# Kernel optimization log

Measured on AMD Instinct MI355X. Metric: run time of the kernel, lower is better.

## Reference

```python
import jax, jax.numpy as jnp
import numpy as np

CLASS_NUM = 4            # number of positive classes
NUM_CLASSES = CLASS_NUM + 1  # last column is the negative class
W_P = 4.0
EPS = 1e-9
THR = 0.5


def setup_inputs() -> dict:
    key = jax.random.key(0)
    k1, k2 = jax.random.split(key)
    N = 4_000_000
    x = jax.random.normal(k1, (N, NUM_CLASSES), dtype=jnp.float32)
    t = jax.random.randint(k2, (N,), 0, NUM_CLASSES)
    return {"x": x, "t": t}


def _conf_mpu_loss(x, t):
    N = x.shape[0]
    p = jax.nn.softmax(x, axis=1)                       # [N, C]
    log_pneg = jnp.log(p[:, -1] + EPS)                  # [N]

    ones = jnp.ones((N,), dtype=jnp.float32)
    counts = jax.ops.segment_sum(ones, t, num_segments=NUM_CLASSES)  # per-class counts
    prior = counts[:CLASS_NUM] / N                      # empirical priors (positive classes)

    # loss_per_class: sum over samples with t==c of -log(p[n,c]+eps)
    logp_t = jnp.log(jnp.take_along_axis(p, t[:, None], axis=1)[:, 0] + EPS)
    class_losses = jax.ops.segment_sum(-logp_t, t, num_segments=NUM_CLASSES)

    # loss_per_class_neg: sum over samples with t==i (i positive) of -log(p_neg+eps)
    loss_neg = jax.ops.segment_sum(-log_pneg, t, num_segments=NUM_CLASSES)[:CLASS_NUM]

    # conf_loss_per_class
    conf = []
    for i in range(CLASS_NUM):
        mask = (p[:, i] > THR) & (t == i)
        nsel = jnp.sum(mask.astype(jnp.float32))
        li = jnp.sum(jnp.where(mask, -log_pneg / p[:, i], 0.0))
        conf.append(li / jnp.maximum(nsel, 1.0))        # li==0 when nsel==0
    mask_n = jnp.all(p <= THR, axis=1) & (t == CLASS_NUM)
    li_n = jnp.sum(jnp.where(mask_n, -log_pneg, 0.0))
    conf_neg = li_n / jnp.maximum(counts[CLASS_NUM], 1.0)  # li_n==0 when no selection
    conf_pos = jnp.stack(conf)                          # [CLASS_NUM]

    denom = jnp.maximum(1.0, counts[:CLASS_NUM])
    risk1 = jnp.sum(prior * class_losses[:CLASS_NUM] / denom)
    risk2 = jnp.sum(prior * conf_pos)
    risk3 = jnp.sum(prior * loss_neg / denom)
    risk4 = conf_neg

    positive_risk = W_P * (risk1 + risk2 - risk3)
    positive_risk = jnp.where(positive_risk < 0, 0.0, positive_risk)
    return positive_risk + risk4


def reference(x, t):
    return _conf_mpu_loss(x, t)
```

## Files before the change

kernel.cpp:

```cpp
#include <hip/hip_runtime.h>

namespace {
constexpr int BLOCK = 256;
constexpr int GRID = 512;
constexpr float WPF = 4.0f;
constexpr float LN2 = 0.69314718056f;
}

__device__ __forceinline__ float wave_reduce(float v) {
#pragma unroll
    for (int o = 32; o > 0; o >>= 1) v += __shfl_down(v, o, 64);
    return v;
}

__global__ __launch_bounds__(BLOCK) void mpu_main(const float* __restrict__ x,
                                                  const int* __restrict__ t,
                                                  float* __restrict__ acc, int N) {
    __shared__ float red[BLOCK / 64][16];

    float S1 = 0.f, S3 = 0.f, li0 = 0.f, li1 = 0.f, li2 = 0.f, li3 = 0.f, liN = 0.f;
    int c0 = 0, c1 = 0, c2 = 0, c3 = 0, n0 = 0, n1 = 0, n2 = 0, n3 = 0;

    auto process = [&](float x0, float x1, float x2, float x3, float x4, int tc) {
        const float mx = fmaxf(fmaxf(fmaxf(x0, x1), fmaxf(x2, x3)), x4);
        const float e0 = __expf(x0 - mx), e1 = __expf(x1 - mx), e2 = __expf(x2 - mx),
                    e3 = __expf(x3 - mx), e4 = __expf(x4 - mx);
        const float sum = ((e0 + e1) + (e2 + e3)) + e4;
        const float base = fmaf(__log2f(sum), LN2, mx);
        const float nln = base - x4;
        const float xt = (tc == 0) ? x0 : (tc == 1) ? x1 : (tc == 2) ? x2
                       : (tc == 3) ? x3 : x4;
        const float nlt = base - xt;
        const bool tpos = (tc < 4);
        const bool sel = (nlt < LN2);
        const bool alle = (sum >= 2.0f);
        const float confv = sel ? nln * __expf(nlt) : 0.f;

        S1 += tpos ? nlt : 0.f;
        S3 += tpos ? nln : 0.f;
        li0 += (tc == 0) ? confv : 0.f;
        li1 += (tc == 1) ? confv : 0.f;
        li2 += (tc == 2) ? confv : 0.f;
        li3 += (tc == 3) ? confv : 0.f;
        liN += (!tpos && alle) ? nln : 0.f;

        const unsigned long long b0 = __ballot(tc == 0);
        const unsigned long long b1 = __ballot(tc == 1);
        const unsigned long long b2 = __ballot(tc == 2);
        const unsigned long long b3 = __ballot(tc == 3);
        const unsigned long long bs = __ballot(sel);
        c0 += (int)__popcll(b0);
        c1 += (int)__popcll(b1);
        c2 += (int)__popcll(b2);
        c3 += (int)__popcll(b3);
        n0 += (int)__popcll(bs & b0);
        n1 += (int)__popcll(bs & b1);
        n2 += (int)__popcll(bs & b2);
        n3 += (int)__popcll(bs & b3);
    };

    auto load_oct = [&](int g, float4 v[10], int4 t2[2]) {
        const float4* xv = reinterpret_cast<const float4*>(x) + (size_t)g * 10;
        const int4* tv = reinterpret_cast<const int4*>(t) + (size_t)g * 2;
#pragma unroll
        for (int j = 0; j < 10; ++j) v[j] = xv[j];
        t2[0] = tv[0];
        t2[1] = tv[1];
    };

    auto process8 = [&](const float4 v[10], const int4 t2[2]) {
        process(v[0].x, v[0].y, v[0].z, v[0].w, v[1].x, t2[0].x);
        process(v[1].y, v[1].z, v[1].w, v[2].x, v[2].y, t2[0].y);
        process(v[2].z, v[2].w, v[3].x, v[3].y, v[3].z, t2[0].z);
        process(v[3].w, v[4].x, v[4].y, v[4].z, v[4].w, t2[0].w);
        process(v[5].x, v[5].y, v[5].z, v[5].w, v[6].x, t2[1].x);
        process(v[6].y, v[6].z, v[6].w, v[7].x, v[7].y, t2[1].y);
        process(v[7].z, v[7].w, v[8].x, v[8].y, v[8].z, t2[1].z);
        process(v[8].w, v[9].x, v[9].y, v[9].z, v[9].w, t2[1].w);
    };

    const int stride = gridDim.x * BLOCK;
    const int nOct = N >> 3;

    int g = blockIdx.x * BLOCK + threadIdx.x;
    float4 cv[10];
    int4 ct[2];
    bool have = (g < nOct);
    if (have) load_oct(g, cv, ct);
    while (have) {
        const int gn = g + stride;
        const bool haveN = (gn < nOct);
        float4 nv[10];
        int4 nt2[2];
        if (haveN) load_oct(gn, nv, nt2);
        process8(cv, ct);
#pragma unroll
        for (int j = 0; j < 10; ++j) cv[j] = nv[j];
        ct[0] = nt2[0];
        ct[1] = nt2[1];
        g = gn;
        have = haveN;
    }

    if (blockIdx.x == 0 && threadIdx.x == 0) {
        for (int k = (N >> 3) << 3; k < N; ++k)
            process(x[k * 5 + 0], x[k * 5 + 1], x[k * 5 + 2], x[k * 5 + 3],
                    x[k * 5 + 4], t[k]);
    }

    const int wv = threadIdx.x >> 6, ln = threadIdx.x & 63;
    float fr[7] = {S1, S3, li0, li1, li2, li3, liN};
#pragma unroll
    for (int j = 0; j < 7; ++j) {
        const float v = wave_reduce(fr[j]);
        if (ln == 0) red[wv][j] = v;
    }
    if (ln == 0) {
        red[wv][7] = (float)c0;  red[wv][8] = (float)c1;
        red[wv][9] = (float)c2;  red[wv][10] = (float)c3;
        red[wv][11] = (float)n0; red[wv][12] = (float)n1;
        red[wv][13] = (float)n2; red[wv][14] = (float)n3;
    }
    __syncthreads();
    if (threadIdx.x < 15) {
        const float v = red[0][threadIdx.x] + red[1][threadIdx.x] +
                        red[2][threadIdx.x] + red[3][threadIdx.x];
        atomicAdd(&acc[threadIdx.x], v);
    }
}

__global__ void mpu_final(const float* __restrict__ acc, float* __restrict__ out, int N) {
    if (threadIdx.x == 0 && blockIdx.x == 0) {
        const float invN = 1.0f / (float)N;
        const float risk1 = acc[0] * invN;
        const float risk3 = acc[1] * invN;
        float risk2 = 0.0f;
#pragma unroll
        for (int i = 0; i < 4; ++i)
            risk2 += (acc[7 + i] * invN) * (acc[2 + i] / fmaxf(acc[11 + i], 1.0f));
        const float c4 = (float)N - (acc[7] + acc[8] + acc[9] + acc[10]);
        const float risk4 = acc[6] / fmaxf(c4, 1.0f);
        float pos = WPF * (risk1 + risk2 - risk3);
        if (pos < 0.0f) pos = 0.0f;
        out[0] = pos + risk4;
    }
}

extern "C" void kernel_launch(void* const* d_in, const int* in_sizes, int n_in,
                              void* d_out, int out_size, void* d_ws, size_t ws_size,
                              hipStream_t stream) {
    const float* x = (const float*)d_in[0];
    const int* t = (const int*)d_in[1];
    float* out = (float*)d_out;
    float* acc = (float*)d_ws;
    const int N = in_sizes[1];

    hipMemsetAsync(acc, 0, 15 * sizeof(float), stream);

    const int nOct = N >> 3;
    int grid = (nOct + BLOCK - 1) / BLOCK;
    if (grid > GRID) grid = GRID;
    if (grid < 1) grid = 1;
    mpu_main<<<grid, BLOCK, 0, stream>>>(x, t, acc, N);
    mpu_final<<<1, 64, 0, stream>>>(acc, out, N);
}
```

Before: 138.3 us.

## Replace register accumulators and ballots with per-class LDS atomic slots

Replaces per-thread accumulators, ballots and wave reductions with shared-memory atomic adds into per-class slots, using 16 replicated copies per wave to spread contention. The math moves to the log2 domain, merges risk1 and risk3 into a single x4-xt sum, and rescales by LN2 at the end. The target logit is fetched with an extra global gather, and the grid cap is doubled. Five LDS atomics per sample plus the gather add substantial traffic compared with the register-based reduction, and the thresholds shift slightly.

Measured after the change: 221.9 us. +60.5%, slower.

```diff
diff --git a/kernel.cpp b/kernel.cpp
--- a/kernel.cpp
+++ b/kernel.cpp
@@ -2,100 +2,92 @@
 
 namespace {
 constexpr int BLOCK = 256;
-constexpr int GRID = 512;
+constexpr int GRID = 1024;
 constexpr float WPF = 4.0f;
-constexpr float LN2 = 0.69314718056f;
-}
-
-__device__ __forceinline__ float wave_reduce(float v) {
-#pragma unroll
-    for (int o = 32; o > 0; o >>= 1) v += __shfl_down(v, o, 64);
-    return v;
+constexpr float LN2 = 0.69314718055994531f;
+constexpr float LOG2E = 1.44269504088896340f;
+constexpr int COPIES = 16;
+constexpr int NREG = (BLOCK / 64) * COPIES;
+constexpr int REGW = 25;
 }
 
 __global__ __launch_bounds__(BLOCK) void mpu_main(const float* __restrict__ x,
                                                   const int* __restrict__ t,
                                                   float* __restrict__ acc, int N) {
-    __shared__ float red[BLOCK / 64][16];
+    __shared__ float slots[NREG * REGW];
+    for (int i = threadIdx.x; i < NREG * REGW; i += BLOCK) slots[i] = 0.0f;
+    __syncthreads();
 
-    float S1 = 0.f, S3 = 0.f, li0 = 0.f, li1 = 0.f, li2 = 0.f, li3 = 0.f, liN = 0.f;
-    int c0 = 0, c1 = 0, c2 = 0, c3 = 0, n0 = 0, n1 = 0, n2 = 0, n3 = 0;
+    const int region = (threadIdx.x >> 6) * COPIES + ((threadIdx.x & 63) >> 2);
+    float* const myslot = &slots[region * REGW];
 
-    auto process = [&](float x0, float x1, float x2, float x3, float x4, int tc) {
-        const float mx = fmaxf(fmaxf(fmaxf(x0, x1), fmaxf(x2, x3)), x4);
-        const float e0 = __expf(x0 - mx), e1 = __expf(x1 - mx), e2 = __expf(x2 - mx),
-                    e3 = __expf(x3 - mx), e4 = __expf(x4 - mx);
-        const float sum = ((e0 + e1) + (e2 + e3)) + e4;
-        const float base = fmaf(__log2f(sum), LN2, mx);
-        const float nln = base - x4;
-        const float xt = (tc == 0) ? x0 : (tc == 1) ? x1 : (tc == 2) ? x2
-                       : (tc == 3) ? x3 : x4;
-        const float nlt = base - xt;
-        const bool tpos = (tc < 4);
-        const bool sel = (nlt < LN2);
-        const bool alle = (sum >= 2.0f);
-        const float confv = sel ? nln * __expf(nlt) : 0.f;
-
-        S1 += tpos ? nlt : 0.f;
-        S3 += tpos ? nln : 0.f;
-        li0 += (tc == 0) ? confv : 0.f;
-        li1 += (tc == 1) ? confv : 0.f;
-        li2 += (tc == 2) ? confv : 0.f;
-        li3 += (tc == 3) ? confv : 0.f;
-        liN += (!tpos && alle) ? nln : 0.f;
-
-        const unsigned long long b0 = __ballot(tc == 0);
-        const unsigned long long b1 = __ballot(tc == 1);
-        const unsigned long long b2 = __ballot(tc == 2);
-        const unsigned long long b3 = __ballot(tc == 3);
-        const unsigned long long bs = __ballot(sel);
-        c0 += (int)__popcll(b0);
-        c1 += (int)__popcll(b1);
-        c2 += (int)__popcll(b2);
-        c3 += (int)__popcll(b3);
-        n0 += (int)__popcll(bs & b0);
-        n1 += (int)__popcll(bs & b1);
-        n2 += (int)__popcll(bs & b2);
-        n3 += (int)__popcll(bs & b3);
+    auto process = [&](float x0, float x1, float x2, float x3, float x4,
+                       float xt, int tc) {
+        const float y0 = x0 * LOG2E, y1 = x1 * LOG2E, y2 = x2 * LOG2E,
+                    y3 = x3 * LOG2E, y4 = x4 * LOG2E;
+        const float f0 = __builtin_amdgcn_exp2f(y0);
+        const float f1 = __builtin_amdgcn_exp2f(y1);
+        const float f2 = __builtin_amdgcn_exp2f(y2);
+        const float f3 = __builtin_amdgcn_exp2f(y3);
+        const float f4 = __builtin_amdgcn_exp2f(y4);
+        const float s = ((f0 + f1) + (f2 + f3)) + f4;
+        const float L2 = __builtin_amdgcn_logf(s);
+        const float thr = L2 - 1.0f;
+        const float yt = xt * LOG2E;
+        const float ymax = fmaxf(fmaxf(fmaxf(y0, y1), fmaxf(y2, y3)), y4);
+        const bool sel = (yt > thr);
+        const bool alle = (ymax <= thr);
+        const float nlnY = L2 - y4;
+        const float cv = nlnY * __builtin_amdgcn_exp2f(L2 - yt);
+        float* const sp = myslot + tc * 5;
+        atomicAdd(sp + 0, 1.0f);
+        atomicAdd(sp + 1, x4 - xt);
+        atomicAdd(sp + 2, sel ? cv : 0.0f);
+        atomicAdd(sp + 3, sel ? 1.0f : 0.0f);
+        atomicAdd(sp + 4, alle ? nlnY : 0.0f);
     };
 
-    auto load_oct = [&](int g, float4 v[10], int4 t2[2]) {
+    auto load_oct = [&](int g, float4 v[10], int4 tt[2]) {
         const float4* xv = reinterpret_cast<const float4*>(x) + (size_t)g * 10;
         const int4* tv = reinterpret_cast<const int4*>(t) + (size_t)g * 2;
 #pragma unroll
         for (int j = 0; j < 10; ++j) v[j] = xv[j];
-        t2[0] = tv[0];
-        t2[1] = tv[1];
-    };
-
-    auto process8 = [&](const float4 v[10], const int4 t2[2]) {
-        process(v[0].x, v[0].y, v[0].z, v[0].w, v[1].x, t2[0].x);
-        process(v[1].y, v[1].z, v[1].w, v[2].x, v[2].y, t2[0].y);
-        process(v[2].z, v[2].w, v[3].x, v[3].y, v[3].z, t2[0].z);
-        process(v[3].w, v[4].x, v[4].y, v[4].z, v[4].w, t2[0].w);
-        process(v[5].x, v[5].y, v[5].z, v[5].w, v[6].x, t2[1].x);
-        process(v[6].y, v[6].z, v[6].w, v[7].x, v[7].y, t2[1].y);
-        process(v[7].z, v[7].w, v[8].x, v[8].y, v[8].z, t2[1].z);
-        process(v[8].w, v[9].x, v[9].y, v[9].z, v[9].w, t2[1].w);
+        tt[0] = tv[0];
+        tt[1] = tv[1];
     };
 
     const int stride = gridDim.x * BLOCK;
     const int nOct = N >> 3;
 
     int g = blockIdx.x * BLOCK + threadIdx.x;
-    float4 cv[10];
+    float4 cv4[10];
     int4 ct[2];
     bool have = (g < nOct);
-    if (have) load_oct(g, cv, ct);
+    if (have) load_oct(g, cv4, ct);
     while (have) {
         const int gn = g + stride;
         const bool haveN = (gn < nOct);
         float4 nv[10];
         int4 nt2[2];
         if (haveN) load_oct(gn, nv, nt2);
-        process8(cv, ct);
+
+        const float* rb = x + (size_t)g * 40;
+        float xt0 = rb[0 + ct[0].x], xt1 = rb[5 + ct[0].y];
+        float xt2 = rb[10 + ct[0].z], xt3 = rb[15 + ct[0].w];
+        float xt4 = rb[20 + ct[1].x], xt5 = rb[25 + ct[1].y];
+        float xt6 = rb[30 + ct[1].z], xt7 = rb[35 + ct[1].w];
+
+        process(cv4[0].x, cv4[0].y, cv4[0].z, cv4[0].w, cv4[1].x, xt0, ct[0].x);
+        process(cv4[1].y, cv4[1].z, cv4[1].w, cv4[2].x, cv4[2].y, xt1, ct[0].y);
+        process(cv4[2].z, cv4[2].w, cv4[3].x, cv4[3].y, cv4[3].z, xt2, ct[0].z);
+        process(cv4[3].w, cv4[4].x, cv4[4].y, cv4[4].z, cv4[4].w, xt3, ct[0].w);
+        process(cv4[5].x, cv4[5].y, cv4[5].z, cv4[5].w, cv4[6].x, xt4, ct[1].x);
+        process(cv4[6].y, cv4[6].z, cv4[6].w, cv4[7].x, cv4[7].y, xt5, ct[1].y);
+        process(cv4[7].z, cv4[7].w, cv4[8].x, cv4[8].y, cv4[8].z, xt6, ct[1].z);
+        process(cv4[8].w, cv4[9].x, cv4[9].y, cv4[9].z, cv4[9].w, xt7, ct[1].w);
+
 #pragma unroll
-        for (int j = 0; j < 10; ++j) cv[j] = nv[j];
+        for (int j = 0; j < 10; ++j) cv4[j] = nv[j];
         ct[0] = nt2[0];
         ct[1] = nt2[1];
         g = gn;
@@ -103,28 +95,18 @@
     }
 
     if (blockIdx.x == 0 && threadIdx.x == 0) {
-        for (int k = (N >> 3) << 3; k < N; ++k)
+        for (int k = (N >> 3) << 3; k < N; ++k) {
+            const int tk = t[k];
             process(x[k * 5 + 0], x[k * 5 + 1], x[k * 5 + 2], x[k * 5 + 3],
-                    x[k * 5 + 4], t[k]);
+                    x[k * 5 + 4], x[k * 5 + tk], tk);
+        }
     }
 
-    const int wv = threadIdx.x >> 6, ln = threadIdx.x & 63;
-    float fr[7] = {S1, S3, li0, li1, li2, li3, liN};
-#pragma unroll
-    for (int j = 0; j < 7; ++j) {
-        const float v = wave_reduce(fr[j]);
-        if (ln == 0) red[wv][j] = v;
-    }
-    if (ln == 0) {
-        red[wv][7] = (float)c0;  red[wv][8] = (float)c1;
-        red[wv][9] = (float)c2;  red[wv][10] = (float)c3;
-        red[wv][11] = (float)n0; red[wv][12] = (float)n1;
-        red[wv][13] = (float)n2; red[wv][14] = (float)n3;
-    }
     __syncthreads();
-    if (threadIdx.x < 15) {
-        const float v = red[0][threadIdx.x] + red[1][threadIdx.x] +
-                        red[2][threadIdx.x] + red[3][threadIdx.x];
+    if (threadIdx.x < REGW) {
+        float v = 0.0f;
+#pragma unroll 8
+        for (int r = 0; r < NREG; ++r) v += slots[r * REGW + threadIdx.x];
         atomicAdd(&acc[threadIdx.x], v);
     }
 }
@@ -132,15 +114,18 @@
 __global__ void mpu_final(const float* __restrict__ acc, float* __restrict__ out, int N) {
     if (threadIdx.x == 0 && blockIdx.x == 0) {
         const float invN = 1.0f / (float)N;
-        const float risk1 = acc[0] * invN;
-        const float risk3 = acc[1] * invN;
+        const float risk13 = (acc[0 * 5 + 1] + acc[1 * 5 + 1] +
+                              acc[2 * 5 + 1] + acc[3 * 5 + 1]) * invN;
         float risk2 = 0.0f;
 #pragma unroll
-        for (int i = 0; i < 4; ++i)
-            risk2 += (acc[7 + i] * invN) * (acc[2 + i] / fmaxf(acc[11 + i], 1.0f));
-        const float c4 = (float)N - (acc[7] + acc[8] + acc[9] + acc[10]);
-        const float risk4 = acc[6] / fmaxf(c4, 1.0f);
-        float pos = WPF * (risk1 + risk2 - risk3);
+        for (int c = 0; c < 4; ++c) {
+            const float cnt = acc[c * 5 + 0];
+            const float li = LN2 * acc[c * 5 + 2];
+            const float nsel = acc[c * 5 + 3];
+            risk2 += (cnt * invN) * (li / fmaxf(nsel, 1.0f));
+        }
+        const float risk4 = LN2 * acc[4 * 5 + 4] / fmaxf(acc[4 * 5 + 0], 1.0f);
+        float pos = WPF * (risk13 + risk2);
         if (pos < 0.0f) pos = 0.0f;
         out[0] = pos + risk4;
     }
@@ -155,7 +140,7 @@
     float* acc = (float*)d_ws;
     const int N = in_sizes[1];
 
-    hipMemsetAsync(acc, 0, 15 * sizeof(float), stream);
+    hipMemsetAsync(acc, 0, REGW * sizeof(float), stream);
 
     const int nOct = N >> 3;
     int grid = (nOct + BLOCK - 1) / BLOCK;
```
